# Optimization experiments

Hardware: AMD Instinct MI355X
Metric: run time of the kernel (lower is better)

## Reference

```python
import jax, jax.numpy as jnp
import numpy as np

B, S, H, N, NREL = 16, 2048, 1024, 128, 8


def setup_inputs() -> dict:
    key = jax.random.key(0)
    ks = jax.random.split(key, 8)
    word_emb = jax.random.normal(ks[0], (B, S, H), dtype=jnp.float32)
    num_ids = jax.random.randint(ks[1], (B, N), 0, S)  # all valid (no -1 padding)
    is_response = jax.random.randint(ks[2], (B, N), 0, 2).astype(jnp.int32)
    numbers = jax.random.normal(ks[3], (B, N), dtype=jnp.float32)
    scale = 1.0 / np.sqrt(H).astype(np.float32)
    w_alpha = jax.random.normal(ks[4], (H, 1), dtype=jnp.float32) * scale
    b_alpha = jnp.zeros((1,), dtype=jnp.float32)
    w_f = jax.random.normal(ks[5], (H, H), dtype=jnp.float32) * scale
    b_f = jnp.zeros((H,), dtype=jnp.float32)
    W_r = jax.random.normal(ks[6], (NREL, H, H), dtype=jnp.float32) * scale  # 8 bias-free relation linears
    return dict(word_emb=word_emb, num_ids=num_ids, is_response=is_response,
                numbers=numbers, w_alpha=w_alpha, b_alpha=b_alpha,
                w_f=w_f, b_f=b_f, W_r=W_r)


def reference(word_emb, num_ids, is_response, numbers, w_alpha, b_alpha, w_f, b_f, W_r):
    Bn, Sn, Hn = word_emb.shape
    Nn = num_ids.shape[1]
    mask = (num_ids >= 0)  # [B,N] valid-node mask (original uses -1 padding)
    idx = jnp.clip(num_ids, 0, Sn - 1)
    # per-batch gather: Init[b,n] = word_emb[b, num_ids[b,n]]  -> [B,N,H]
    Init = jnp.take_along_axis(word_emb, idx[:, :, None], axis=1)
    alpha = jax.nn.sigmoid(Init @ w_alpha + b_alpha)  # [B,N,1]
    # all 8 relation transforms of every sender node j: T[b,r,j,:] = Init[b,j] @ W_r[r].T
    T = jnp.einsum('bnh,rkh->brnk', Init, W_r)  # [B,8,N,H]
    # relation id r(b,i,j) = 4*(num_i>num_j) + 2*resp_i + resp_j
    gt = (numbers[:, :, None] > numbers[:, None, :]).astype(jnp.int32)  # [B,N,N]
    resp = (is_response == 1).astype(jnp.int32)
    R = 4 * gt + 2 * resp[:, :, None] + resp[:, None, :]  # [B,N,N]
    sel = jax.nn.one_hot(R, NREL, dtype=word_emb.dtype)  # [B,N,N,8]
    not_diag = ~jnp.eye(Nn, dtype=bool)
    # edge weight over sender j: alpha_j, valid i & j, i != j
    wgt = (alpha[:, None, :, 0] * mask[:, None, :] * mask[:, :, None]
           * not_diag[None]).astype(word_emb.dtype)  # [B,N,N]
    Temp = jnp.einsum('bijr,brjh->bih', sel * wgt[..., None], T)  # [B,N,H]
    n_nodes = mask.sum(axis=1)  # [B]
    denom = jnp.maximum(n_nodes - 1, 1).astype(word_emb.dtype)
    Temp = Temp / denom[:, None, None]
    out = jax.nn.relu(Init @ w_f + b_f + Temp)  # [B,N,H]
    return out
```

## Files before the change

kernel.cpp:

```cpp
#include <hip/hip_runtime.h>
#include <hip/hip_bf16.h>
#include <stdint.h>

#define B_ 16
#define S_ 2048
#define H_ 1024
#define N_ 128
#define M_ (B_*N_)
#define K5 5120
#define MP 2176

typedef __attribute__((ext_vector_type(8))) short s8vec;
typedef __attribute__((ext_vector_type(4))) short s4vec;
typedef __attribute__((ext_vector_type(4))) float f4vec;
typedef __hip_bfloat16 bf16;

__global__ void k_sort(const int* __restrict__ num_ids, const int* __restrict__ is_resp,
                       const float* __restrict__ numbers,
                       int* __restrict__ sigma, int* __restrict__ newgrp,
                       int* __restrict__ respv, float* __restrict__ denom) {
    int b = blockIdx.x, i = threadIdx.x;
    __shared__ float nums[N_];
    __shared__ int sig[N_];
    __shared__ int cnt;
    float ni = numbers[b*N_ + i];
    int idv = num_ids[b*N_ + i];
    int valid = (idv >= 0) ? 1 : 0;
    nums[i] = ni;
    if (i == 0) cnt = 0;
    __syncthreads();
    int p = 0;
    for (int j = 0; j < N_; ++j) {
        float nj = nums[j];
        p += (nj < ni || (nj == ni && j < i)) ? 1 : 0;
    }
    sig[p] = i;
    atomicAdd(&cnt, valid);
    __syncthreads();
    sigma[b*N_ + i] = sig[i];
    int cur = sig[i];
    int prv = (i > 0) ? sig[i-1] : 0;
    newgrp[b*N_ + i] = (i == 0 || nums[cur] != nums[prv]) ? 1 : 0;
    respv[b*N_ + i] = ((is_resp[b*N_ + i] == 1) ? 1 : 0) | (valid << 1);
    if (i == 0) denom[b] = fmaxf((float)(cnt - 1), 1.0f);
}

__global__ void k_meta(const int* __restrict__ respv, int* __restrict__ aperm,
                       int* __restrict__ iperm, int* __restrict__ meta) {
    __shared__ int s0[1024], s1[1024];
    int t = threadIdx.x;
    aperm[t] = -1; aperm[t + 1024] = -1;
    if (t < MP - 2048) aperm[t + 2048] = -1;
    int r0 = 2*t, r1 = 2*t + 1;
    int c_a = respv[r0] & 1, c_b = respv[r1] & 1;
    int a0 = 1 - c_a, b0 = 1 - c_b;
    s0[t] = a0 + b0;
    s1[t] = c_a + c_b;
    __syncthreads();
    for (int off = 1; off < 1024; off <<= 1) {
        int v0 = (t >= off) ? s0[t-off] : 0;
        int v1 = (t >= off) ? s1[t-off] : 0;
        __syncthreads();
        s0[t] += v0; s1[t] += v1;
        __syncthreads();
    }
    int C0 = s0[1023], C1 = s1[1023];
    int P0 = ((C0 + 127) >> 7) << 7;
    int ex0 = s0[t] - (a0 + b0);
    int ex1 = s1[t] - (c_a + c_b);
    int p_a = (c_a == 0) ? ex0 : P0 + ex1;
    int p_b = (c_b == 0) ? ex0 + a0 : P0 + ex1 + c_a;
    aperm[p_a] = r0; iperm[r0] = p_a;
    aperm[p_b] = r1; iperm[r1] = p_b;
    if (t == 0) { meta[0] = P0; meta[1] = C0; meta[2] = C1; }
}

__global__ void k_gather(const float* __restrict__ word_emb, const int* __restrict__ num_ids,
                         const float* __restrict__ w_alpha, const float* __restrict__ b_alpha,
                         const float* __restrict__ denom, const int* __restrict__ iperm,
                         bf16* __restrict__ A, float* __restrict__ ascaled) {
    int blk = blockIdx.x;
    int b = blk >> 7, n = blk & 127;
    int t = threadIdx.x;
    int idv = num_ids[b*N_ + n];
    int valid = (idv >= 0) ? 1 : 0;
    int idx = idv < 0 ? 0 : (idv > S_-1 ? S_-1 : idv);
    int pr = iperm[b*N_ + n];
    const float4* row = (const float4*)(word_emb + ((size_t)b*S_ + idx)*H_);
    float4 v = row[t];
    float4 w = ((const float4*)w_alpha)[t];
    float part = v.x*w.x + v.y*w.y + v.z*w.z + v.w*w.w;
    union { s4vec v4; bf16 h[4]; } pk;
    pk.h[0] = __float2bfloat16(v.x);
    pk.h[1] = __float2bfloat16(v.y);
    pk.h[2] = __float2bfloat16(v.z);
    pk.h[3] = __float2bfloat16(v.w);
    *(s4vec*)(A + (size_t)pr*K5 + 4*H_ + t*4) = pk.v4;
#pragma unroll
    for (int off = 32; off > 0; off >>= 1) part += __shfl_down(part, off, 64);
    __shared__ float red[4];
    if ((t & 63) == 0) red[t >> 6] = part;
    __syncthreads();
    if (t == 0) {
        float dot = red[0] + red[1] + red[2] + red[3] + b_alpha[0];
        float al = 1.0f / (1.0f + __expf(-dot));
        ascaled[b*N_ + n] = valid ? (al / denom[b]) : 0.0f;
    }
}

__global__ void k_wtf(const float* __restrict__ W_r, const float* __restrict__ w_f,
                      bf16* __restrict__ Wt) {
    __shared__ float lds[64][65];
    int bid = blockIdx.x;
    int t = threadIdx.x;
    if (bid < 4096) {
        size_t o = ((size_t)bid*256 + t)*8;
        int cs = (int)(o >> 20);
        int c = cs >> 2, s = cs & 3;
        int r = ((s >> 1) << 2) + 2*c + (s & 1);
        size_t off = o & (size_t)(H_*H_ - 1);
        const float4* src = (const float4*)(W_r + (size_t)r*H_*H_ + off);
        float4 v0 = src[0], v1 = src[1];
        union { s8vec v8; bf16 h[8]; } pk;
        pk.h[0] = __float2bfloat16(v0.x); pk.h[1] = __float2bfloat16(v0.y);
        pk.h[2] = __float2bfloat16(v0.z); pk.h[3] = __float2bfloat16(v0.w);
        pk.h[4] = __float2bfloat16(v1.x); pk.h[5] = __float2bfloat16(v1.y);
        pk.h[6] = __float2bfloat16(v1.z); pk.h[7] = __float2bfloat16(v1.w);
        *(s8vec*)(Wt + (size_t)(c*5 + s)*H_*H_ + off) = pk.v8;
        return;
    }
    int bb = bid - 4096;
    int bi = bb & 15, bj = bb >> 4;
    int ty = t >> 4, tx = t & 15;
#pragma unroll
    for (int i = 0; i < 4; ++i) {
        int r = ty*4 + i;
        float4 v = *(const float4*)(w_f + (size_t)(bi*64 + r)*H_ + bj*64 + tx*4);
        lds[r][tx*4+0] = v.x; lds[r][tx*4+1] = v.y;
        lds[r][tx*4+2] = v.z; lds[r][tx*4+3] = v.w;
    }
    __syncthreads();
    bf16* d0 = Wt + (size_t)4*H_*H_;
    bf16* d1 = Wt + (size_t)9*H_*H_;
#pragma unroll
    for (int i = 0; i < 4; ++i) {
        int n = ty*4 + i;
        size_t doff = (size_t)(bj*64 + n)*H_ + bi*64 + tx*4;
        union { s4vec v4; bf16 h[4]; } pk;
#pragma unroll
        for (int j = 0; j < 4; ++j) pk.h[j] = __float2bfloat16(lds[tx*4+j][n]);
        *(s4vec*)(d0 + doff) = pk.v4;
        *(s4vec*)(d1 + doff) = pk.v4;
    }
}

__global__ void k_build(const float* __restrict__ ascaled, const int* __restrict__ sigma,
                        const int* __restrict__ newgrp, const int* __restrict__ respv,
                        const int* __restrict__ iperm, bf16* __restrict__ A) {
    int b = blockIdx.y;
    int h = blockIdx.x*64 + threadIdx.x;
    __shared__ float as_s[N_];
    __shared__ int sig_s[N_], ng_s[N_], rv_s[N_], pm_s[N_];
    for (int j = threadIdx.x; j < N_; j += 64) {
        as_s[j] = ascaled[b*N_ + j];
        sig_s[j] = sigma[b*N_ + j];
        ng_s[j] = newgrp[b*N_ + j];
        rv_s[j] = respv[b*N_ + j];
        pm_s[j] = iperm[b*N_ + j];
    }
    __syncthreads();
    const bf16* initcol = A + 4*H_ + h;
    float tot0 = 0.f, tot1 = 0.f;
#pragma unroll 8
    for (int i2 = 0; i2 < N_; ++i2) {
        float v = as_s[i2] * __bfloat162float(initcol[(size_t)pm_s[i2]*K5]);
        if (rv_s[i2] & 1) tot1 += v; else tot0 += v;
    }
    float cS0=0.f, cS1=0.f, cG0=0.f, cG1=0.f;
#pragma unroll 8
    for (int p = 0; p < N_; ++p) {
        int i2 = sig_s[p];
        if (ng_s[p]) { cS0 += cG0; cS1 += cG1; cG0 = 0.f; cG1 = 0.f; }
        float v = as_s[i2] * __bfloat162float(initcol[(size_t)pm_s[i2]*K5]);
        int resp = rv_s[i2] & 1;
        float vf = (rv_s[i2] >> 1) ? 1.0f : 0.0f;
        float G0 = cS0, G1 = cS1;
        float L0 = tot0 - G0 - (resp ? 0.f : v);
        float L1 = tot1 - G1 - (resp ? v : 0.f);
        bf16* Ar = A + (size_t)pm_s[i2]*K5 + h;
        Ar[0*H_] = __float2bfloat16(L0*vf);
        Ar[1*H_] = __float2bfloat16(L1*vf);
        Ar[2*H_] = __float2bfloat16(G0*vf);
        Ar[3*H_] = __float2bfloat16(G1*vf);
        if (resp) cG1 += v; else cG0 += v;
    }
}

#define BM 64
#define BN 64
#define BK 64
#define NSTEP (K5/BK)

__global__ __launch_bounds__(256, 3) void k_gemm(const bf16* __restrict__ A,
                                                 const bf16* __restrict__ Wt,
                                                 const int* __restrict__ meta,
                                                 const int* __restrict__ aperm,
                                                 const float* __restrict__ b_f,
                                                 float* __restrict__ out) {
    __shared__ __align__(16) bf16 As0[BM*BK], As1[BM*BK], As2[BM*BK];
    __shared__ __align__(16) bf16 Bs0[BN*BK], Bs1[BN*BK], Bs2[BN*BK];
    int tid = threadIdx.x;
    int w = tid >> 6, lane = tid & 63;
    int q = lane >> 4, r = lane & 15;
    int bid = blockIdx.x;
    int wg = (bid & 7)*68 + (bid >> 3);
    int mt = wg % 34, nt = wg / 34;
    int rowBase = mt * BM, colBase = nt * BN;
    int wm = w >> 1, wn = w & 1;
    int P0 = meta[0];
    const bf16* Wtc = Wt + ((rowBase >= P0) ? (size_t)5*H_*H_ : 0);

    int og[2][4];
    float bias[2];
#pragma unroll
    for (int mi = 0; mi < 2; ++mi) {
        int rb = rowBase + wm*32 + mi*16 + q*4;
#pragma unroll
        for (int e = 0; e < 4; ++e) og[mi][e] = aperm[rb + e];
    }
#pragma unroll
    for (int ni = 0; ni < 2; ++ni) bias[ni] = b_f[colBase + wn*32 + ni*16 + r];
#pragma unroll
    for (int mi = 0; mi < 2; ++mi)
#pragma unroll
        for (int e = 0; e < 4; ++e) asm volatile("" : "+v"(og[mi][e]));
    asm volatile("" : "+v"(bias[0]), "+v"(bias[1]));

    f4vec acc[2][2];
#pragma unroll
    for (int mi = 0; mi < 2; ++mi)
#pragma unroll
        for (int ni = 0; ni < 2; ++ni)
#pragma unroll
            for (int e = 0; e < 4; ++e) acc[mi][ni][e] = 0.0f;

    auto STAGE = [&](bf16* AsB, bf16* BsB, int kin) {
        int slot = kin >> 10, koff = kin & 1023;
        const bf16* Wslot = Wtc + ((size_t)slot << 20);
#pragma unroll
        for (int j = 0; j < 2; ++j) {
            int c = tid + j*256;
            int row = c >> 3;
            int p = (c & 7) ^ (row & 7);
            const bf16* ga = A + (size_t)(rowBase + row)*K5 + kin + p*8;
            __builtin_amdgcn_global_load_lds((const __attribute__((address_space(1))) void*)ga,
                (__attribute__((address_space(3))) void*)((char*)AsB + j*4096 + w*1024), 16, 0, 0);
            const bf16* gb = Wslot + ((size_t)(colBase + row) << 10) + koff + p*8;
            __builtin_amdgcn_global_load_lds((const __attribute__((address_space(1))) void*)gb,
                (__attribute__((address_space(3))) void*)((char*)BsB + j*4096 + w*1024), 16, 0, 0);
        }
    };

    auto COMPUTE = [&](const bf16* AsB, const bf16* BsB) {
        const short* Asp = (const short*)AsB;
        const short* Bsp = (const short*)BsB;
        s8vec af[2][2], bfr[2][2];
#pragma unroll
        for (int kk = 0; kk < 2; ++kk) {
            int sl = ((kk*4 + q) ^ (r & 7)) << 3;
#pragma unroll
            for (int mi = 0; mi < 2; ++mi)
                af[kk][mi] = *(const s8vec*)(Asp + (wm*32 + mi*16 + r)*BK + sl);
#pragma unroll
            for (int ni = 0; ni < 2; ++ni)
                bfr[kk][ni] = *(const s8vec*)(Bsp + (wn*32 + ni*16 + r)*BK + sl);
        }
#pragma unroll
        for (int kk = 0; kk < 2; ++kk)
#pragma unroll
            for (int mi = 0; mi < 2; ++mi)
#pragma unroll
                for (int ni = 0; ni < 2; ++ni)
                    acc[mi][ni] = __builtin_amdgcn_mfma_f32_16x16x32_bf16(
                        af[kk][mi], bfr[kk][ni], acc[mi][ni], 0, 0, 0);
    };

    STAGE(As0, Bs0, 0);
    STAGE(As1, Bs1, BK);
    bf16 *cA = As0, *cB = Bs0;
    bf16 *nA = As1, *nB = Bs1;
    bf16 *sA = As2, *sB = Bs2;
    for (int t = 0; t < NSTEP; ++t) {
        if (t + 1 < NSTEP) asm volatile("s_waitcnt vmcnt(4)" ::: "memory");
        else               asm volatile("s_waitcnt vmcnt(0)" ::: "memory");
        __builtin_amdgcn_s_barrier();
        __builtin_amdgcn_sched_barrier(0);
        if (t + 2 < NSTEP) STAGE(sA, sB, (t + 2)*BK);
        COMPUTE(cA, cB);
        bf16* tA = cA; cA = nA; nA = sA; sA = tA;
        bf16* tB = cB; cB = nB; nB = sB; sB = tB;
    }

#pragma unroll
    for (int mi = 0; mi < 2; ++mi) {
#pragma unroll
        for (int ni = 0; ni < 2; ++ni) {
            int cc = colBase + wn*32 + ni*16 + r;
            if (og[mi][0] >= 0) out[(size_t)og[mi][0]*H_ + cc] = fmaxf(acc[mi][ni][0] + bias[ni], 0.0f);
            if (og[mi][1] >= 0) out[(size_t)og[mi][1]*H_ + cc] = fmaxf(acc[mi][ni][1] + bias[ni], 0.0f);
            if (og[mi][2] >= 0) out[(size_t)og[mi][2]*H_ + cc] = fmaxf(acc[mi][ni][2] + bias[ni], 0.0f);
            if (og[mi][3] >= 0) out[(size_t)og[mi][3]*H_ + cc] = fmaxf(acc[mi][ni][3] + bias[ni], 0.0f);
        }
    }
}

extern "C" void kernel_launch(void* const* d_in, const int* in_sizes, int n_in,
                              void* d_out, int out_size, void* d_ws, size_t ws_size,
                              hipStream_t stream) {
    (void)in_sizes; (void)n_in; (void)out_size; (void)ws_size;
    const float* word_emb = (const float*)d_in[0];
    const int*   num_ids  = (const int*)d_in[1];
    const int*   is_resp  = (const int*)d_in[2];
    const float* numbers  = (const float*)d_in[3];
    const float* w_alpha  = (const float*)d_in[4];
    const float* b_alpha  = (const float*)d_in[5];
    const float* w_f      = (const float*)d_in[6];
    const float* b_f      = (const float*)d_in[7];
    const float* W_r      = (const float*)d_in[8];
    float* out = (float*)d_out;

    char* ws = (char*)d_ws;
    bf16*  Aws     = (bf16*)(ws);
    bf16*  Wt      = (bf16*)(ws + 22282240);
    float* ascaled = (float*)(ws + 52166656);
    int*   sigma   = (int*)(ws + 52174848);
    int*   newgrp  = (int*)(ws + 52183040);
    int*   respv   = (int*)(ws + 52191232);
    float* denom   = (float*)(ws + 52199424);
    int*   aperm   = (int*)(ws + 52199488);
    int*   iperm   = (int*)(ws + 52208192);
    int*   meta    = (int*)(ws + 52216384);

    k_sort  <<<16,   128, 0, stream>>>(num_ids, is_resp, numbers, sigma, newgrp, respv, denom);
    k_meta  <<<1,   1024, 0, stream>>>(respv, aperm, iperm, meta);
    k_gather<<<2048, 256, 0, stream>>>(word_emb, num_ids, w_alpha, b_alpha, denom, iperm,
                                       Aws, ascaled);
    k_wtf   <<<4352, 256, 0, stream>>>(W_r, w_f, Wt);
    k_build <<<dim3(16,16), 64, 0, stream>>>(ascaled, sigma, newgrp, respv, iperm, Aws);
    k_gemm  <<<544,  256, 0, stream>>>(Aws, Wt, meta, aperm, b_f, out);
}
```

Before: 322.4 us.

## Merge gather and weight-convert kernels; switch GEMM to double buffering with higher occupancy

Combines the gather/alpha kernel and the weight bf16 conversion kernel into a single launch, which removes one launch and lets the two independent memory-bound jobs run side by side. The GEMM drops from a three-stage LDS ring to two buffers and raises the launch-bounds occupancy target from three to four waves per SIMD. Prefetch for the next tile is issued before compute, followed by a full vmcnt(0) wait and a barrier. This trades prefetch depth for occupancy, and the shallower pipeline may expose global load latency.

```diff
diff --git a/kernel.cpp b/kernel.cpp
--- a/kernel.cpp
+++ b/kernel.cpp
@@ -75,46 +75,44 @@
     if (t == 0) { meta[0] = P0; meta[1] = C0; meta[2] = C1; }
 }
 
-__global__ void k_gather(const float* __restrict__ word_emb, const int* __restrict__ num_ids,
-                         const float* __restrict__ w_alpha, const float* __restrict__ b_alpha,
-                         const float* __restrict__ denom, const int* __restrict__ iperm,
-                         bf16* __restrict__ A, float* __restrict__ ascaled) {
-    int blk = blockIdx.x;
-    int b = blk >> 7, n = blk & 127;
-    int t = threadIdx.x;
-    int idv = num_ids[b*N_ + n];
-    int valid = (idv >= 0) ? 1 : 0;
-    int idx = idv < 0 ? 0 : (idv > S_-1 ? S_-1 : idv);
-    int pr = iperm[b*N_ + n];
-    const float4* row = (const float4*)(word_emb + ((size_t)b*S_ + idx)*H_);
-    float4 v = row[t];
-    float4 w = ((const float4*)w_alpha)[t];
-    float part = v.x*w.x + v.y*w.y + v.z*w.z + v.w*w.w;
-    union { s4vec v4; bf16 h[4]; } pk;
-    pk.h[0] = __float2bfloat16(v.x);
-    pk.h[1] = __float2bfloat16(v.y);
-    pk.h[2] = __float2bfloat16(v.z);
-    pk.h[3] = __float2bfloat16(v.w);
-    *(s4vec*)(A + (size_t)pr*K5 + 4*H_ + t*4) = pk.v4;
-#pragma unroll
-    for (int off = 32; off > 0; off >>= 1) part += __shfl_down(part, off, 64);
-    __shared__ float red[4];
-    if ((t & 63) == 0) red[t >> 6] = part;
-    __syncthreads();
-    if (t == 0) {
-        float dot = red[0] + red[1] + red[2] + red[3] + b_alpha[0];
-        float al = 1.0f / (1.0f + __expf(-dot));
-        ascaled[b*N_ + n] = valid ? (al / denom[b]) : 0.0f;
-    }
-}
-
-__global__ void k_wtf(const float* __restrict__ W_r, const float* __restrict__ w_f,
-                      bf16* __restrict__ Wt) {
+__global__ void k_prep(const float* __restrict__ word_emb, const int* __restrict__ num_ids,
+                       const float* __restrict__ w_alpha, const float* __restrict__ b_alpha,
+                       const float* __restrict__ denom, const int* __restrict__ iperm,
+                       const float* __restrict__ W_r, const float* __restrict__ w_f,
+                       bf16* __restrict__ A, float* __restrict__ ascaled,
+                       bf16* __restrict__ Wt) {
     __shared__ float lds[64][65];
     int bid = blockIdx.x;
     int t = threadIdx.x;
-    if (bid < 4096) {
-        size_t o = ((size_t)bid*256 + t)*8;
+    if (bid < 2048) {
+        int b = bid >> 7, n = bid & 127;
+        int idv = num_ids[b*N_ + n];
+        int valid = (idv >= 0) ? 1 : 0;
+        int idx = idv < 0 ? 0 : (idv > S_-1 ? S_-1 : idv);
+        int pr = iperm[b*N_ + n];
+        const float4* row = (const float4*)(word_emb + ((size_t)b*S_ + idx)*H_);
+        float4 v = row[t];
+        float4 w = ((const float4*)w_alpha)[t];
+        float part = v.x*w.x + v.y*w.y + v.z*w.z + v.w*w.w;
+        union { s4vec v4; bf16 h[4]; } pk;
+        pk.h[0] = __float2bfloat16(v.x);
+        pk.h[1] = __float2bfloat16(v.y);
+        pk.h[2] = __float2bfloat16(v.z);
+        pk.h[3] = __float2bfloat16(v.w);
+        *(s4vec*)(A + (size_t)pr*K5 + 4*H_ + t*4) = pk.v4;
+#pragma unroll
+        for (int off = 32; off > 0; off >>= 1) part += __shfl_down(part, off, 64);
+        if ((t & 63) == 0) lds[0][t >> 6] = part;
+        __syncthreads();
+        if (t == 0) {
+            float dot = lds[0][0] + lds[0][1] + lds[0][2] + lds[0][3] + b_alpha[0];
+            float al = 1.0f / (1.0f + __expf(-dot));
+            ascaled[b*N_ + n] = valid ? (al / denom[b]) : 0.0f;
+        }
+        return;
+    }
+    if (bid < 6144) {
+        size_t o = ((size_t)(bid - 2048)*256 + t)*8;
         int cs = (int)(o >> 20);
         int c = cs >> 2, s = cs & 3;
         int r = ((s >> 1) << 2) + 2*c + (s & 1);
@@ -129,7 +127,7 @@
         *(s8vec*)(Wt + (size_t)(c*5 + s)*H_*H_ + off) = pk.v8;
         return;
     }
-    int bb = bid - 4096;
+    int bb = bid - 6144;
     int bi = bb & 15, bj = bb >> 4;
     int ty = t >> 4, tx = t & 15;
 #pragma unroll
@@ -201,14 +199,14 @@
 #define BK 64
 #define NSTEP (K5/BK)
 
-__global__ __launch_bounds__(256, 3) void k_gemm(const bf16* __restrict__ A,
+__global__ __launch_bounds__(256, 4) void k_gemm(const bf16* __restrict__ A,
                                                  const bf16* __restrict__ Wt,
                                                  const int* __restrict__ meta,
                                                  const int* __restrict__ aperm,
                                                  const float* __restrict__ b_f,
                                                  float* __restrict__ out) {
-    __shared__ __align__(16) bf16 As0[BM*BK], As1[BM*BK], As2[BM*BK];
-    __shared__ __align__(16) bf16 Bs0[BN*BK], Bs1[BN*BK], Bs2[BN*BK];
+    __shared__ __align__(16) bf16 As0[BM*BK], As1[BM*BK];
+    __shared__ __align__(16) bf16 Bs0[BN*BK], Bs1[BN*BK];
     int tid = threadIdx.x;
     int w = tid >> 6, lane = tid & 63;
     int q = lane >> 4, r = lane & 15;
@@ -286,19 +284,19 @@
     };
 
     STAGE(As0, Bs0, 0);
-    STAGE(As1, Bs1, BK);
-    bf16 *cA = As0, *cB = Bs0;
-    bf16 *nA = As1, *nB = Bs1;
-    bf16 *sA = As2, *sB = Bs2;
+    asm volatile("s_waitcnt vmcnt(0)" ::: "memory");
+    __builtin_amdgcn_s_barrier();
+    __builtin_amdgcn_sched_barrier(0);
+
+    bf16 *cA = As0, *cB = Bs0, *nA = As1, *nB = Bs1;
     for (int t = 0; t < NSTEP; ++t) {
-        if (t + 1 < NSTEP) asm volatile("s_waitcnt vmcnt(4)" ::: "memory");
-        else               asm volatile("s_waitcnt vmcnt(0)" ::: "memory");
+        if (t + 1 < NSTEP) STAGE(nA, nB, (t + 1)*BK);
+        COMPUTE(cA, cB);
+        asm volatile("s_waitcnt vmcnt(0)" ::: "memory");
         __builtin_amdgcn_s_barrier();
         __builtin_amdgcn_sched_barrier(0);
-        if (t + 2 < NSTEP) STAGE(sA, sB, (t + 2)*BK);
-        COMPUTE(cA, cB);
-        bf16* tA = cA; cA = nA; nA = sA; sA = tA;
-        bf16* tB = cB; cB = nB; nB = sB; sB = tB;
+        bf16* tA = cA; cA = nA; nA = tA;
+        bf16* tB = cB; cB = nB; nB = tB;
     }
 
 #pragma unroll
@@ -343,9 +341,8 @@
 
     k_sort  <<<16,   128, 0, stream>>>(num_ids, is_resp, numbers, sigma, newgrp, respv, denom);
     k_meta  <<<1,   1024, 0, stream>>>(respv, aperm, iperm, meta);
-    k_gather<<<2048, 256, 0, stream>>>(word_emb, num_ids, w_alpha, b_alpha, denom, iperm,
-                                       Aws, ascaled);
-    k_wtf   <<<4352, 256, 0, stream>>>(W_r, w_f, Wt);
+    k_prep  <<<6400, 256, 0, stream>>>(word_emb, num_ids, w_alpha, b_alpha, denom, iperm,
+                                       W_r, w_f, Aws, ascaled, Wt);
     k_build <<<dim3(16,16), 64, 0, stream>>>(ascaled, sigma, newgrp, respv, iperm, Aws);
     k_gemm  <<<544,  256, 0, stream>>>(Aws, Wt, meta, aperm, b_f, out);
 }
```

After: 319.2 us. No clear change (-1.0%).
